# Kernel optimization log

Measured on AMD Instinct MI355X. Metric: run time of the kernel, lower is better.

Reference implementation:

```python
import jax, jax.numpy as jnp
import numpy as np


def squash(x, axis=-1):
    # norm_sq/(1+norm_sq) * x/norm, exactly as the torch version
    norm_sq = jnp.sum(x * x, axis=axis, keepdims=True)
    norm = jnp.sqrt(norm_sq)
    return norm_sq / (1.0 + norm_sq) * (x / norm)


def setup_inputs() -> dict:
    key = jax.random.key(0)
    k1, k2 = jax.random.split(key)
    batch, in_caps, in_hid, out_caps, out_hid = 128, 1152, 16, 32, 16
    input_capsules = jax.random.normal(k1, (batch, in_caps, in_hid), dtype=jnp.float32)
    # EinMix weight: 'in_caps in_hid out_caps out_hid'
    W = jax.random.normal(k2, (in_caps, in_hid, out_caps, out_hid), dtype=jnp.float32) * 0.05
    return {"input_capsules": input_capsules, "W": W, "routing_iterations": 3}


def reference(input_capsules, W, routing_iterations):
    # U: [batch, in_caps, out_caps, out_hid]
    U = jnp.einsum('bih,ihoj->bioj', input_capsules, W)
    batch, in_caps, out_caps, out_hid = U.shape
    B = jnp.zeros((batch, in_caps, out_caps), dtype=U.dtype)
    V = None
    for _ in range(routing_iterations):
        C = jax.nn.softmax(B, axis=-1)           # [b, i, o]
        S = jnp.einsum('bio,bioh->boh', C, U)    # [b, o, h]
        V = squash(S, axis=-1)                   # [b, o, h]
        B = B + jnp.einsum('bioh,boh->bio', U, V)
    return V
```

## Files before the change

kernel.cpp:

```cpp
#include <hip/hip_runtime.h>
#include <hip/hip_bf16.h>


#define IN_CAPS 1152
#define OUT_CAPS 32
#define BATCH 128
#define IPC 18
#define NBLK_I (IN_CAPS / IPC)
#define SV_ELEMS (BATCH * OUT_CAPS * 16)

typedef __attribute__((ext_vector_type(8))) short short8;
typedef __attribute__((ext_vector_type(4))) float f32x4;

__device__ inline unsigned f2bf(float x) {
  unsigned u = __builtin_bit_cast(unsigned, x);
  return (u + 0x7FFFu + ((u >> 16) & 1u)) >> 16;
}

__global__ __launch_bounds__(256) void conv_w(const float* __restrict__ W,
                                              unsigned short* __restrict__ Wb) {
  __shared__ float st[16 * 516];
  const int t = threadIdx.x;
  const size_t ibase = (size_t)blockIdx.x * 8192;
  const float4* src = (const float4*)(W + ibase);
#pragma unroll
  for (int r = 0; r < 8; ++r) {
    const int f = r * 256 + t;
    const int k = f >> 7, c4 = f & 127;
    *(float4*)&st[k * 516 + c4 * 4] = src[f];
  }
  __syncthreads();
  unsigned short* dst = Wb + ibase;
#pragma unroll
  for (int r = 0; r < 4; ++r) {
    const int u = r * 256 + t;
    const int o = u >> 5, l = u & 31;
    const int col = o * 16 + (l & 15), k0 = (l >> 4) * 8;
    unsigned b[8];
#pragma unroll
    for (int j = 0; j < 8; ++j) b[j] = f2bf(st[(k0 + j) * 516 + col]);
    uint4 outv;
    outv.x = b[0] | (b[1] << 16);
    outv.y = b[2] | (b[3] << 16);
    outv.z = b[4] | (b[5] << 16);
    outv.w = b[6] | (b[7] << 16);
    *(uint4*)(dst + (size_t)u * 8) = outv;
  }
}

__device__ __forceinline__ void build_xs(const float* __restrict__ X, int bg,
                                         int i0, int t, unsigned (*xs)[64][4]) {
#pragma unroll
  for (int rep = 0; rep < IPC * 256 / 512; ++rep) {
    const int base = rep * 512 + t;
    const int ii = base >> 8;
    const int e = base & 255;
    const int l2 = e >> 2, ju = e & 3;
    unsigned val = 0;
    if (l2 < 32) {
      const float2 f = *(const float2*)(X +
          ((size_t)(bg * 16 + (l2 & 15)) * IN_CAPS + (i0 + ii)) * 16 +
          (l2 >> 4) * 8 + 2 * ju);
      val = f2bf(f.x) | (f2bf(f.y) << 16);
    }
    xs[ii][l2][ju] = val;
  }
}

__device__ __forceinline__ short8 ld_x(const unsigned (*xs)[64][4], int ii, int l) {
  return __builtin_bit_cast(short8, *(const uint4*)(&xs[ii][l][0]));
}

__global__ __launch_bounds__(512, 4)
void caps_pass1(const unsigned short* __restrict__ Wb,
                const float* __restrict__ X, float* __restrict__ P) {
  __shared__ __align__(16) unsigned xs[IPC][64][4];
  const int t = threadIdx.x, w = t >> 6, l = t & 63;
  const int q = l >> 4, bl = l & 15;
  const int gx = blockIdx.x, iblk = gx & 63, bg = gx >> 6;
  const int i0 = iblk * IPC;

  build_xs(X, bg, i0, t, xs);
  __syncthreads();

  const short8* wp = (const short8*)Wb + ((size_t)i0 * 32 + w * 4) * 32 + (l & 31);
  f32x4 sacc[4];
#pragma unroll
  for (int m = 0; m < 4; ++m) sacc[m] = (f32x4){0.f, 0.f, 0.f, 0.f};

  for (int ii = 0; ii < IPC; ++ii) {
    short8 x = ld_x(xs, ii, l);
    short8 a0 = wp[0], a1 = wp[32], a2 = wp[64], a3 = wp[96];
    wp += 1024;
    sacc[0] = __builtin_amdgcn_mfma_f32_16x16x32_bf16(a0, x, sacc[0], 0, 0, 0);
    sacc[1] = __builtin_amdgcn_mfma_f32_16x16x32_bf16(a1, x, sacc[1], 0, 0, 0);
    sacc[2] = __builtin_amdgcn_mfma_f32_16x16x32_bf16(a2, x, sacc[2], 0, 0, 0);
    sacc[3] = __builtin_amdgcn_mfma_f32_16x16x32_bf16(a3, x, sacc[3], 0, 0, 0);
  }
  float* pp = P + ((size_t)iblk * 128 + bg * 16 + bl) * 512 + w * 64 + q * 4;
#pragma unroll
  for (int m = 0; m < 4; ++m) *(f32x4*)(pp + m * 16) = sacc[m] * (1.f / 32.f);
}

__global__ __launch_bounds__(512, 4)
void caps_pass23(const unsigned short* __restrict__ Wb,
                 const float* __restrict__ X,
                 const float* __restrict__ Vt,
                 float* __restrict__ P) {
  __shared__ __align__(16) unsigned xs[IPC][64][4];
  __shared__ float part[2][8][16];
  const int t = threadIdx.x, w = t >> 6, l = t & 63;
  const int q = l >> 4, bl = l & 15;
  const int gx = blockIdx.x, iblk = gx & 63, bg = gx >> 6;
  const int i0 = iblk * IPC;

  f32x4 v[4], sacc[4];
#pragma unroll
  for (int m = 0; m < 4; ++m) {
    v[m] = ((const f32x4*)Vt)[((size_t)(bg * 8 + w) * 64 + l) * 4 + m];
    sacc[m] = (f32x4){0.f, 0.f, 0.f, 0.f};
  }

  build_xs(X, bg, i0, t, xs);
  __syncthreads();

  const short8* wp = (const short8*)Wb + ((size_t)i0 * 32 + w * 4) * 32 + (l & 31);
  short8 an[4];
  short8 xn = ld_x(xs, 0, l);
#pragma unroll
  for (int m = 0; m < 4; ++m) an[m] = wp[m * 32];
  wp += 1024;

  for (int ii = 0; ii < IPC; ++ii) {
    short8 ac[4];
#pragma unroll
    for (int m = 0; m < 4; ++m) ac[m] = an[m];
    short8 xc = xn;
    if (ii + 1 < IPC) {
      xn = ld_x(xs, ii + 1, l);
#pragma unroll
      for (int m = 0; m < 4; ++m) an[m] = wp[m * 32];
      wp += 1024;
    }

    const f32x4 z = {0.f, 0.f, 0.f, 0.f};
    f32x4 d[4];
#pragma unroll
    for (int m = 0; m < 4; ++m)
      d[m] = __builtin_amdgcn_mfma_f32_16x16x32_bf16(ac[m], xc, z, 0, 0, 0);

    float e[4];
#pragma unroll
    for (int m = 0; m < 4; ++m) {
      f32x4 pr = d[m] * v[m];
      float p = (pr[0] + pr[1]) + (pr[2] + pr[3]);
      p += __shfl_xor(p, 16);
      p += __shfl_xor(p, 32);
      e[m] = __expf(p);
    }
    const float esum = (e[0] + e[1]) + (e[2] + e[3]);
    if (q == 0) part[ii & 1][w][bl] = esum;
    __syncthreads();
    float den = 0.f;
#pragma unroll
    for (int ww = 0; ww < 8; ++ww) den += part[ii & 1][ww][bl];
    const float rden = __builtin_amdgcn_rcpf(den);
#pragma unroll
    for (int m = 0; m < 4; ++m) sacc[m] += d[m] * (e[m] * rden);
  }

  float* pp = P + ((size_t)iblk * 128 + bg * 16 + bl) * 512 + w * 64 + q * 4;
#pragma unroll
  for (int m = 0; m < 4; ++m) *(f32x4*)(pp + m * 16) = sacc[m];
}

template <int MODE>
__global__ __launch_bounds__(256)
void reduce_squash(const float* __restrict__ P, float* __restrict__ Vt,
                   float* __restrict__ V1p, float* __restrict__ Out) {
  const int j = blockIdx.x * 256 + threadIdx.x;
  float s = 0.f;
  const float* p = P + j;
#pragma unroll 8
  for (int k = 0; k < NBLK_I; ++k) s += p[(size_t)k * SV_ELEMS];
  float ns = s * s;
  ns += __shfl_xor(ns, 1);
  ns += __shfl_xor(ns, 2);
  ns += __shfl_xor(ns, 4);
  ns += __shfl_xor(ns, 8);
  const float sc = ns / ((1.f + ns) * sqrtf(ns));
  float vv = s * sc;
  if constexpr (MODE == 2) {
    Out[j] = vv;
  } else {
    if constexpr (MODE == 0) V1p[j] = vv;
    if constexpr (MODE == 1) vv += V1p[j];
    const int b = j >> 9, oh = j & 511, o = oh >> 4, h = oh & 15;
    const int bg = b >> 4, bl = b & 15, w = o >> 2, m = o & 3, qq = h >> 2;
    Vt[(((size_t)(bg * 8 + w) * 64 + qq * 16 + bl) * 16) + m * 4 + (h & 3)] = vv;
  }
}

extern "C" void kernel_launch(void* const* d_in, const int* in_sizes, int n_in,
                              void* d_out, int out_size, void* d_ws, size_t ws_size,
                              hipStream_t stream) {
  const float* X  = (const float*)d_in[0];
  const float* Wg = (const float*)d_in[1];

  float* P   = (float*)d_ws;
  float* Vt  = P + (size_t)NBLK_I * SV_ELEMS;
  float* V1p = Vt + SV_ELEMS;
  unsigned short* Wb = (unsigned short*)(V1p + SV_ELEMS);
  float* out = (float*)d_out;

  conv_w<<<IN_CAPS, 256, 0, stream>>>(Wg, Wb);

  caps_pass1<<<512, 512, 0, stream>>>(Wb, X, P);
  reduce_squash<0><<<256, 256, 0, stream>>>(P, Vt, V1p, nullptr);

  caps_pass23<<<512, 512, 0, stream>>>(Wb, X, Vt, P);
  reduce_squash<1><<<256, 256, 0, stream>>>(P, Vt, V1p, nullptr);

  caps_pass23<<<512, 512, 0, stream>>>(Wb, X, Vt, P);
  reduce_squash<2><<<256, 256, 0, stream>>>(P, nullptr, nullptr, out);
}
```

Measured before the change: 165.1 us.

## Replace partial-sum buffers and reduce kernels with atomic accumulation and fused squash

Each routing pass now accumulates its per-block partial S directly into a global S buffer with float atomics, replacing the 64-way partial buffer and the separate reduce_squash kernels. The squash of the previous iterations' S is recomputed inside the consumer pass. The final squash runs in a last-block-done epilogue driven by an atomic counter. Zeroing of the accumulators and counter is folded into the weight-conversion kernel. This removes three launches and the large partial-buffer write/read traffic, at the cost of many contended float atomics and nondeterministic summation order.

```diff
diff --git a/kernel.cpp b/kernel.cpp
--- a/kernel.cpp
+++ b/kernel.cpp
@@ -3,11 +3,9 @@
 
 
 #define IN_CAPS 1152
-#define OUT_CAPS 32
-#define BATCH 128
 #define IPC 18
-#define NBLK_I (IN_CAPS / IPC)
-#define SV_ELEMS (BATCH * OUT_CAPS * 16)
+#define NBLK_I 64
+#define SV_ELEMS 65536
 
 typedef __attribute__((ext_vector_type(8))) short short8;
 typedef __attribute__((ext_vector_type(4))) float f32x4;
@@ -17,10 +15,16 @@
   return (u + 0x7FFFu + ((u >> 16) & 1u)) >> 16;
 }
 
-__global__ __launch_bounds__(256) void conv_w(const float* __restrict__ W,
-                                              unsigned short* __restrict__ Wb) {
+__global__ __launch_bounds__(256)
+void conv_w(const float* __restrict__ W, unsigned short* __restrict__ Wb,
+            float* __restrict__ Szero, unsigned* __restrict__ counter) {
   __shared__ float st[16 * 516];
   const int t = threadIdx.x;
+  if (blockIdx.x < 192) {
+    ((float4*)Szero)[blockIdx.x * 256 + t] = make_float4(0.f, 0.f, 0.f, 0.f);
+  }
+  if (blockIdx.x == 192 && t < 16) counter[t] = 0u;
+
   const size_t ibase = (size_t)blockIdx.x * 8192;
   const float4* src = (const float4*)(W + ibase);
 #pragma unroll
@@ -51,7 +55,7 @@
 __device__ __forceinline__ void build_xs(const float* __restrict__ X, int bg,
                                          int i0, int t, unsigned (*xs)[64][4]) {
 #pragma unroll
-  for (int rep = 0; rep < IPC * 256 / 512; ++rep) {
+  for (int rep = 0; rep < (IPC * 256) / 512; ++rep) {
     const int base = rep * 512 + t;
     const int ii = base >> 8;
     const int e = base & 255;
@@ -71,133 +75,135 @@
   return __builtin_bit_cast(short8, *(const uint4*)(&xs[ii][l][0]));
 }
 
+__device__ __forceinline__ f32x4 vfrag(const float* __restrict__ Srow, int m) {
+  f32x4 s4 = *(const f32x4*)(Srow + m * 16);
+  float ns = (s4[0] * s4[0] + s4[1] * s4[1]) + (s4[2] * s4[2] + s4[3] * s4[3]);
+  ns += __shfl_xor(ns, 16);
+  ns += __shfl_xor(ns, 32);
+  const float sc = ns / ((1.f + ns) * sqrtf(ns));
+  return s4 * sc;
+}
+
+template <int PASS>
 __global__ __launch_bounds__(512, 4)
-void caps_pass1(const unsigned short* __restrict__ Wb,
-                const float* __restrict__ X, float* __restrict__ P) {
+void caps_pass(const unsigned short* __restrict__ Wb,
+               const float* __restrict__ X,
+               const float* __restrict__ S1, const float* __restrict__ S2,
+               float* __restrict__ Scur, unsigned* __restrict__ counter,
+               float* __restrict__ Out) {
   __shared__ __align__(16) unsigned xs[IPC][64][4];
+  __shared__ float part[2][8][16];
+  __shared__ unsigned lastFlag;
+
   const int t = threadIdx.x, w = t >> 6, l = t & 63;
   const int q = l >> 4, bl = l & 15;
-  const int gx = blockIdx.x, iblk = gx & 63, bg = gx >> 6;
+  const int bx = blockIdx.x, iblk = bx & 63, bg = bx >> 6;
   const int i0 = iblk * IPC;
+
+  f32x4 v[4], sacc[4];
+#pragma unroll
+  for (int m = 0; m < 4; ++m) sacc[m] = (f32x4){0.f, 0.f, 0.f, 0.f};
+  if constexpr (PASS >= 2) {
+    const size_t rbase = ((size_t)(bg * 16 + bl) * 32 + w * 4) * 16 + q * 4;
+#pragma unroll
+    for (int m = 0; m < 4; ++m) {
+      v[m] = vfrag(S1 + rbase, m);
+      if constexpr (PASS == 3) v[m] += vfrag(S2 + rbase, m);
+    }
+  }
 
   build_xs(X, bg, i0, t, xs);
   __syncthreads();
 
   const short8* wp = (const short8*)Wb + ((size_t)i0 * 32 + w * 4) * 32 + (l & 31);
-  f32x4 sacc[4];
-#pragma unroll
-  for (int m = 0; m < 4; ++m) sacc[m] = (f32x4){0.f, 0.f, 0.f, 0.f};
-
-  for (int ii = 0; ii < IPC; ++ii) {
-    short8 x = ld_x(xs, ii, l);
-    short8 a0 = wp[0], a1 = wp[32], a2 = wp[64], a3 = wp[96];
+
+  if constexpr (PASS == 1) {
+    for (int ii = 0; ii < IPC; ++ii) {
+      short8 x = ld_x(xs, ii, l);
+      short8 a0 = wp[0], a1 = wp[32], a2 = wp[64], a3 = wp[96];
+      wp += 1024;
+      sacc[0] = __builtin_amdgcn_mfma_f32_16x16x32_bf16(a0, x, sacc[0], 0, 0, 0);
+      sacc[1] = __builtin_amdgcn_mfma_f32_16x16x32_bf16(a1, x, sacc[1], 0, 0, 0);
+      sacc[2] = __builtin_amdgcn_mfma_f32_16x16x32_bf16(a2, x, sacc[2], 0, 0, 0);
+      sacc[3] = __builtin_amdgcn_mfma_f32_16x16x32_bf16(a3, x, sacc[3], 0, 0, 0);
+    }
+  } else {
+    short8 an[4];
+    short8 xn = ld_x(xs, 0, l);
+#pragma unroll
+    for (int m = 0; m < 4; ++m) an[m] = wp[m * 32];
     wp += 1024;
-    sacc[0] = __builtin_amdgcn_mfma_f32_16x16x32_bf16(a0, x, sacc[0], 0, 0, 0);
-    sacc[1] = __builtin_amdgcn_mfma_f32_16x16x32_bf16(a1, x, sacc[1], 0, 0, 0);
-    sacc[2] = __builtin_amdgcn_mfma_f32_16x16x32_bf16(a2, x, sacc[2], 0, 0, 0);
-    sacc[3] = __builtin_amdgcn_mfma_f32_16x16x32_bf16(a3, x, sacc[3], 0, 0, 0);
-  }
-  float* pp = P + ((size_t)iblk * 128 + bg * 16 + bl) * 512 + w * 64 + q * 4;
-#pragma unroll
-  for (int m = 0; m < 4; ++m) *(f32x4*)(pp + m * 16) = sacc[m] * (1.f / 32.f);
-}
-
-__global__ __launch_bounds__(512, 4)
-void caps_pass23(const unsigned short* __restrict__ Wb,
-                 const float* __restrict__ X,
-                 const float* __restrict__ Vt,
-                 float* __restrict__ P) {
-  __shared__ __align__(16) unsigned xs[IPC][64][4];
-  __shared__ float part[2][8][16];
-  const int t = threadIdx.x, w = t >> 6, l = t & 63;
-  const int q = l >> 4, bl = l & 15;
-  const int gx = blockIdx.x, iblk = gx & 63, bg = gx >> 6;
-  const int i0 = iblk * IPC;
-
-  f32x4 v[4], sacc[4];
-#pragma unroll
-  for (int m = 0; m < 4; ++m) {
-    v[m] = ((const f32x4*)Vt)[((size_t)(bg * 8 + w) * 64 + l) * 4 + m];
-    sacc[m] = (f32x4){0.f, 0.f, 0.f, 0.f};
-  }
-
-  build_xs(X, bg, i0, t, xs);
-  __syncthreads();
-
-  const short8* wp = (const short8*)Wb + ((size_t)i0 * 32 + w * 4) * 32 + (l & 31);
-  short8 an[4];
-  short8 xn = ld_x(xs, 0, l);
-#pragma unroll
-  for (int m = 0; m < 4; ++m) an[m] = wp[m * 32];
-  wp += 1024;
-
-  for (int ii = 0; ii < IPC; ++ii) {
-    short8 ac[4];
-#pragma unroll
-    for (int m = 0; m < 4; ++m) ac[m] = an[m];
-    short8 xc = xn;
-    if (ii + 1 < IPC) {
-      xn = ld_x(xs, ii + 1, l);
-#pragma unroll
-      for (int m = 0; m < 4; ++m) an[m] = wp[m * 32];
-      wp += 1024;
-    }
-
-    const f32x4 z = {0.f, 0.f, 0.f, 0.f};
-    f32x4 d[4];
-#pragma unroll
-    for (int m = 0; m < 4; ++m)
-      d[m] = __builtin_amdgcn_mfma_f32_16x16x32_bf16(ac[m], xc, z, 0, 0, 0);
-
-    float e[4];
-#pragma unroll
-    for (int m = 0; m < 4; ++m) {
-      f32x4 pr = d[m] * v[m];
-      float p = (pr[0] + pr[1]) + (pr[2] + pr[3]);
-      p += __shfl_xor(p, 16);
-      p += __shfl_xor(p, 32);
-      e[m] = __expf(p);
-    }
-    const float esum = (e[0] + e[1]) + (e[2] + e[3]);
-    if (q == 0) part[ii & 1][w][bl] = esum;
+
+    for (int ii = 0; ii < IPC; ++ii) {
+      short8 ac[4];
+#pragma unroll
+      for (int m = 0; m < 4; ++m) ac[m] = an[m];
+      short8 xc = xn;
+      if (ii + 1 < IPC) {
+        xn = ld_x(xs, ii + 1, l);
+#pragma unroll
+        for (int m = 0; m < 4; ++m) an[m] = wp[m * 32];
+        wp += 1024;
+      }
+
+      const f32x4 z = {0.f, 0.f, 0.f, 0.f};
+      f32x4 d[4];
+#pragma unroll
+      for (int m = 0; m < 4; ++m)
+        d[m] = __builtin_amdgcn_mfma_f32_16x16x32_bf16(ac[m], xc, z, 0, 0, 0);
+
+      float e[4];
+#pragma unroll
+      for (int m = 0; m < 4; ++m) {
+        f32x4 pr = d[m] * v[m];
+        float p = (pr[0] + pr[1]) + (pr[2] + pr[3]);
+        p += __shfl_xor(p, 16);
+        p += __shfl_xor(p, 32);
+        e[m] = __expf(p);
+      }
+      const float esum = (e[0] + e[1]) + (e[2] + e[3]);
+      if (q == 0) part[ii & 1][w][bl] = esum;
+      __syncthreads();
+      float den = 0.f;
+#pragma unroll
+      for (int ww = 0; ww < 8; ++ww) den += part[ii & 1][ww][bl];
+      const float rden = __builtin_amdgcn_rcpf(den);
+#pragma unroll
+      for (int m = 0; m < 4; ++m) sacc[m] += d[m] * (e[m] * rden);
+    }
+  }
+
+  float* sp = Scur + ((size_t)(bg * 16 + bl) * 512) + w * 64 + q * 4;
+#pragma unroll
+  for (int m = 0; m < 4; ++m)
+#pragma unroll
+    for (int r = 0; r < 4; ++r) {
+      float val = sacc[m][r];
+      if constexpr (PASS == 1) val *= (1.f / 32.f);
+      atomicAdd(sp + m * 16 + r, val);
+    }
+
+  if constexpr (PASS == 3) {
+    __threadfence();
     __syncthreads();
-    float den = 0.f;
-#pragma unroll
-    for (int ww = 0; ww < 8; ++ww) den += part[ii & 1][ww][bl];
-    const float rden = __builtin_amdgcn_rcpf(den);
-#pragma unroll
-    for (int m = 0; m < 4; ++m) sacc[m] += d[m] * (e[m] * rden);
-  }
-
-  float* pp = P + ((size_t)iblk * 128 + bg * 16 + bl) * 512 + w * 64 + q * 4;
-#pragma unroll
-  for (int m = 0; m < 4; ++m) *(f32x4*)(pp + m * 16) = sacc[m];
-}
-
-template <int MODE>
-__global__ __launch_bounds__(256)
-void reduce_squash(const float* __restrict__ P, float* __restrict__ Vt,
-                   float* __restrict__ V1p, float* __restrict__ Out) {
-  const int j = blockIdx.x * 256 + threadIdx.x;
-  float s = 0.f;
-  const float* p = P + j;
-#pragma unroll 8
-  for (int k = 0; k < NBLK_I; ++k) s += p[(size_t)k * SV_ELEMS];
-  float ns = s * s;
-  ns += __shfl_xor(ns, 1);
-  ns += __shfl_xor(ns, 2);
-  ns += __shfl_xor(ns, 4);
-  ns += __shfl_xor(ns, 8);
-  const float sc = ns / ((1.f + ns) * sqrtf(ns));
-  float vv = s * sc;
-  if constexpr (MODE == 2) {
-    Out[j] = vv;
-  } else {
-    if constexpr (MODE == 0) V1p[j] = vv;
-    if constexpr (MODE == 1) vv += V1p[j];
-    const int b = j >> 9, oh = j & 511, o = oh >> 4, h = oh & 15;
-    const int bg = b >> 4, bl = b & 15, w = o >> 2, m = o & 3, qq = h >> 2;
-    Vt[(((size_t)(bg * 8 + w) * 64 + qq * 16 + bl) * 16) + m * 4 + (h & 3)] = vv;
+    if (t == 0) lastFlag = (atomicAdd(counter, 1u) == 511u) ? 1u : 0u;
+    __syncthreads();
+    if (lastFlag) {
+      __threadfence();
+#pragma unroll
+      for (int rr = 0; rr < 8; ++rr) {
+        const int row = rr * 512 + t;
+        const f32x4* s = (const f32x4*)(Scur + (size_t)row * 16);
+        f32x4 s0 = s[0], s1 = s[1], s2 = s[2], s3 = s[3];
+        float ns = (s0[0]*s0[0]+s0[1]*s0[1]+s0[2]*s0[2]+s0[3]*s0[3])
+                 + (s1[0]*s1[0]+s1[1]*s1[1]+s1[2]*s1[2]+s1[3]*s1[3])
+                 + (s2[0]*s2[0]+s2[1]*s2[1]+s2[2]*s2[2]+s2[3]*s2[3])
+                 + (s3[0]*s3[0]+s3[1]*s3[1]+s3[2]*s3[2]+s3[3]*s3[3]);
+        const float sc = ns / ((1.f + ns) * sqrtf(ns));
+        f32x4* op = (f32x4*)(Out + (size_t)row * 16);
+        op[0] = s0 * sc; op[1] = s1 * sc; op[2] = s2 * sc; op[3] = s3 * sc;
+      }
+    }
   }
 }
 
@@ -207,20 +213,15 @@
   const float* X  = (const float*)d_in[0];
   const float* Wg = (const float*)d_in[1];
 
-  float* P   = (float*)d_ws;
-  float* Vt  = P + (size_t)NBLK_I * SV_ELEMS;
-  float* V1p = Vt + SV_ELEMS;
-  unsigned short* Wb = (unsigned short*)(V1p + SV_ELEMS);
+  float* S1 = (float*)d_ws;
+  float* S2 = S1 + SV_ELEMS;
+  float* S3 = S2 + SV_ELEMS;
+  unsigned* counter = (unsigned*)(S3 + SV_ELEMS);
+  unsigned short* Wb = (unsigned short*)(S1 + 196672);
   float* out = (float*)d_out;
 
-  conv_w<<<IN_CAPS, 256, 0, stream>>>(Wg, Wb);
-
-  caps_pass1<<<512, 512, 0, stream>>>(Wb, X, P);
-  reduce_squash<0><<<256, 256, 0, stream>>>(P, Vt, V1p, nullptr);
-
-  caps_pass23<<<512, 512, 0, stream>>>(Wb, X, Vt, P);
-  reduce_squash<1><<<256, 256, 0, stream>>>(P, Vt, V1p, nullptr);
-
-  caps_pass23<<<512, 512, 0, stream>>>(Wb, X, Vt, P);
-  reduce_squash<2><<<256, 256, 0, stream>>>(P, nullptr, nullptr, out);
-}
+  conv_w<<<IN_CAPS, 256, 0, stream>>>(Wg, Wb, S1, counter);
+  caps_pass<1><<<512, 512, 0, stream>>>(Wb, X, nullptr, nullptr, S1, nullptr, nullptr);
+  caps_pass<2><<<512, 512, 0, stream>>>(Wb, X, S1, nullptr, S2, nullptr, nullptr);
+  caps_pass<3><<<512, 512, 0, stream>>>(Wb, X, S1, S2, S3, counter, out);
+}
```

After: 427.2 us. 159% more time.
